# Optimization experiments

Hardware: AMD Instinct MI355X
Metric: run time of the kernel (lower is better)

The kernel has to match this reference:

```python
import jax, jax.numpy as jnp
import numpy as np

N = 100000
E = 1600000
IN_DIM, HID_DIM, OUT_DIM = 128, 64, 128


def glorot(key, shape):
    lim = float(np.sqrt(6.0 / (shape[0] + shape[1])))
    return jax.random.uniform(key, shape, jnp.float32, -lim, lim)


def setup_inputs() -> dict:
    key = jax.random.key(0)
    k1, k2, k3, k4, k5 = jax.random.split(key, 5)
    x = jax.random.normal(k1, (N, IN_DIM), jnp.float32)
    edge_index = jax.random.randint(k2, (2, E), 0, N, jnp.int64)
    edge_weight = jax.random.uniform(k3, (E,), jnp.float32)
    W1 = glorot(k4, (IN_DIM, HID_DIM))
    b1 = jnp.zeros((HID_DIM,), jnp.float32)
    W2 = glorot(k5, (HID_DIM, OUT_DIM))
    b2 = jnp.zeros((OUT_DIM,), jnp.float32)
    return {"x": x, "edge_index": edge_index, "edge_weight": edge_weight,
            "W1": W1, "b1": b1, "W2": W2, "b2": b2}


def gcn_norm(edge_index, edge_weight, num_nodes):
    # add self-loops with weight 1 (PyG GCNConv default)
    loops = jnp.arange(num_nodes, dtype=edge_index.dtype)
    row = jnp.concatenate([edge_index[0], loops])
    col = jnp.concatenate([edge_index[1], loops])
    w = jnp.concatenate([edge_weight, jnp.ones((num_nodes,), edge_weight.dtype)])
    deg = jax.ops.segment_sum(w, col, num_segments=num_nodes)  # in-degree of targets
    dinv = jnp.where(deg > 0, jax.lax.rsqrt(deg), 0.0)
    norm = dinv[row] * w * dinv[col]  # [E+N]
    return row, col, norm


def gcn_conv(x, row, col, norm, W, b, num_nodes):
    h = x @ W                                   # [N, D_out]
    msg = h[row] * norm[:, None]                # [E+N, D_out] gather + scale
    out = jax.ops.segment_sum(msg, col, num_segments=num_nodes)  # scatter-add
    return out + b


def reference(x, edge_index, edge_weight, W1, b1, W2, b2):
    row, col, norm = gcn_norm(edge_index, edge_weight, N)
    h = jax.nn.relu(gcn_conv(x, row, col, norm, W1, b1, N))
    out = gcn_conv(h, row, col, norm, W2, b2, N)
    return out
```

## Files before the change

### kernel.cpp

```cpp
#include <hip/hip_runtime.h>
#include <hip/hip_bf16.h>

typedef __hip_bfloat16 bf16;
typedef __attribute__((ext_vector_type(8))) short short8;
typedef __attribute__((ext_vector_type(4))) float f32x4;
typedef __attribute__((ext_vector_type(2))) unsigned uv2;
typedef __attribute__((ext_vector_type(4))) unsigned uv4;
union V8 { uint4 u; short8 v; };

__device__ __forceinline__ float bf2f(bf16 v) { return __bfloat162float(v); }
__device__ __forceinline__ float lo16(unsigned u) { return __uint_as_float((u & 0xffffu) << 16); }
__device__ __forceinline__ float hi16(unsigned u) { return __uint_as_float(u & 0xffff0000u); }
__device__ __forceinline__ unsigned short f2bfbits(float f) {
    return (unsigned short)(__hip_bfloat16_raw(__float2bfloat16(f)).x);
}
__device__ __forceinline__ unsigned pack2(float a, float b) {
    return (unsigned)f2bfbits(a) | ((unsigned)f2bfbits(b) << 16);
}

__device__ __forceinline__ float ldf(const void* p, size_t i, bool isbf) {
    return isbf ? bf2f(((const bf16*)p)[i]) : ((const float*)p)[i];
}
__device__ __forceinline__ int ldi(const void* p, size_t i, bool is64) {
    return is64 ? (int)((const long long*)p)[i] : ((const int*)p)[i];
}
__device__ __forceinline__ float sane(float v) {
    return (v == v && fabsf(v) < 1e30f) ? v : 0.f;
}

__device__ __forceinline__ uint2 nt_ld2(const uint2* p) {
    uv2 v = __builtin_nontemporal_load((const uv2*)p);
    return make_uint2(v.x, v.y);
}
__device__ __forceinline__ void nt_st4(uint4* p, uint4 v) {
    uv4 t; t.x = v.x; t.y = v.y; t.z = v.z; t.w = v.w;
    __builtin_nontemporal_store(t, (uv4*)p);
}

#define DC_CNT_SHIFT 44
#define DC_FIX_MASK  0xFFFFFFFFFFFULL
#define DC_FIX_SCALE 4194304.0f

__global__ void initk(unsigned long long* __restrict__ dc, int* __restrict__ hist,
                      int* __restrict__ bcnt, int n, int initdc,
                      const unsigned* __restrict__ w1w, const unsigned* __restrict__ eiw,
                      int* __restrict__ flags) {
    int i = blockIdx.x * blockDim.x + threadIdx.x;
    if (initdc && i < n) dc[i] = (unsigned long long)(1u << 22);
    if (i < 256) { hist[i] = 0; bcnt[i] = 0; }
    if (blockIdx.x == 0) {
        __shared__ int cnt[2];
        if (threadIdx.x < 2) cnt[threadIdx.x] = 0;
        __syncthreads();
        int c0 = 0;
        for (int j = threadIdx.x; j < 4096; j += 256) {
            unsigned u = w1w[j];
            unsigned e0 = (u >> 7) & 0xFFu, e1 = (u >> 23) & 0xFFu;
            if (e0 <= 125u && e1 <= 125u) c0++;
        }
        int c1 = 0;
        for (int j = threadIdx.x; j < 2048; j += 256)
            if (eiw[2 * j + 1] == 0u) c1++;
        atomicAdd(&cnt[0], c0);
        atomicAdd(&cnt[1], c1);
        __syncthreads();
        if (threadIdx.x == 0) {
            flags[0] = (cnt[0] >= 3072) ? 1 : 0;
            flags[1] = (cnt[1] >= 1024) ? 1 : 0;
        }
    }
}

__global__ void degcnt(const void* __restrict__ ei, const void* __restrict__ w,
                       unsigned long long* __restrict__ dc,
                       const int* __restrict__ flags, int e, int n) {
    const bool isbf = flags[0] != 0;
    const bool is64 = flags[1] != 0;
    int i = blockIdx.x * blockDim.x + threadIdx.x;
    if (i < e) {
        int c = ldi(ei, (size_t)e + i, is64);
        if ((unsigned)c < (unsigned)n) {
            float wv = sane(ldf(w, i, isbf));
            wv = fminf(fmaxf(wv, 0.f), 1024.f);
            unsigned long long pk = (1ULL << DC_CNT_SHIFT)
                                  + (unsigned long long)llrintf(wv * DC_FIX_SCALE);
            atomicAdd(&dc[c], pk);
        }
    }
}

__global__ __launch_bounds__(1024) void binA(const void* __restrict__ ei,
                                             const void* __restrict__ w,
                                             int* __restrict__ bcnt,
                                             uint2* __restrict__ stage,
                                             const int* __restrict__ flags,
                                             int e, int n, int k, int cap) {
    __shared__ uint2 recs[4096];
    __shared__ unsigned tgt[4096];
    __shared__ int lh[256], loff[256], lbase[256];
    const bool isbf = flags[0] != 0;
    const bool is64 = flags[1] != 0;
    const int t = threadIdx.x;
    if (t < 256) lh[t] = 0;
    __syncthreads();

    int b_[4], lr_[4], valid_[4];
    uint2 rec_[4];
    const int base = blockIdx.x * 4096;
#pragma unroll
    for (int u = 0; u < 4; ++u) {
        int i = base + u * 1024 + t;
        valid_[u] = 0;
        if (i < e) {
            int r = ldi(ei, (size_t)i, is64);
            int c = ldi(ei, (size_t)e + i, is64);
            if ((unsigned)c < (unsigned)n) {
                bool rv = (unsigned)r < (unsigned)n;
                float wv = rv ? sane(ldf(w, i, isbf)) : 0.f;
                int b = c >> k;
                unsigned cloc = (unsigned)(c - (b << k));
                rec_[u] = make_uint2((cloc << 20) | (rv ? (unsigned)r : 0u),
                                     __float_as_uint(wv));
                b_[u] = b;
                lr_[u] = atomicAdd(&lh[b], 1);
                valid_[u] = 1;
            }
        }
    }
    __syncthreads();

    if (t < 256) loff[t] = lh[t];
    __syncthreads();
    for (int off = 1; off < 256; off <<= 1) {
        int v = 0;
        if (t < 256 && t >= off) v = loff[t - off];
        __syncthreads();
        if (t < 256 && t >= off) loff[t] += v;
        __syncthreads();
    }
    if (t < 256) {
        int c = lh[t];
        loff[t] -= c;
        lbase[t] = (c > 0) ? atomicAdd(&bcnt[t], c) : 0;
    }
    __syncthreads();

#pragma unroll
    for (int u = 0; u < 4; ++u)
        if (valid_[u]) {
            int slot = loff[b_[u]] + lr_[u];
            recs[slot] = rec_[u];
            unsigned gi = (unsigned)(lbase[b_[u]] + lr_[u]);
            tgt[slot] = (gi < (unsigned)cap)
                          ? (unsigned)b_[u] * (unsigned)cap + gi
                          : 0xFFFFFFFFu;
        }
    __syncthreads();

    const int total = loff[255] + lh[255];
    for (int s = t; s < total; s += 1024) {
        unsigned g = tgt[s];
        if (g != 0xFFFFFFFFu) stage[g] = recs[s];
    }
}

__global__ __launch_bounds__(1024) void degcntB(const uint2* __restrict__ stage,
                                                const int* __restrict__ bcnt,
                                                unsigned long long* __restrict__ dc,
                                                int n, int k, int cap) {
    __shared__ unsigned long long dcl[4096];
    const int b  = blockIdx.x;
    const int lo = b << k;
    const int hi = min(n, lo + (1 << k));
    const int bs = hi - lo;
    const int t  = threadIdx.x;
    for (int j = t; j < bs; j += 1024)
        dcl[j] = (unsigned long long)(1u << 22);
    __syncthreads();
    const uint2* sb = stage + (size_t)b * cap;
    const int cnt_b = min(bcnt[b], cap);
    for (int s = t; s < cnt_b; s += 1024) {
        uint2 rec = sb[s];
        int cloc  = (int)(rec.x >> 20);
        float wv  = __uint_as_float(rec.y);
        wv = fminf(fmaxf(wv, 0.f), 1024.f);
        unsigned long long pk = (1ULL << DC_CNT_SHIFT)
                              + (unsigned long long)llrintf(wv * DC_FIX_SCALE);
        atomicAdd(&dcl[cloc], pk);
    }
    __syncthreads();
    for (int j = t; j < bs; j += 1024) dc[lo + j] = dcl[j];
}

__global__ __launch_bounds__(1024) void scan1(const unsigned long long* __restrict__ dc,
                                              int* __restrict__ rp,
                                              int* __restrict__ bsum, int n) {
    __shared__ int s[1024];
    int gid = blockIdx.x * 1024 + threadIdx.x;
    int v = (gid < n) ? (int)(dc[gid] >> DC_CNT_SHIFT) : 0;
    s[threadIdx.x] = v;
    __syncthreads();
    for (int off = 1; off < 1024; off <<= 1) {
        int t = 0;
        if (threadIdx.x >= off) t = s[threadIdx.x - off];
        __syncthreads();
        if (threadIdx.x >= off) s[threadIdx.x] += t;
        __syncthreads();
    }
    if (gid < n) rp[gid] = s[threadIdx.x] - v;
    if (threadIdx.x == 1023) bsum[blockIdx.x] = s[1023];
}

__global__ __launch_bounds__(1024) void scan2(const int* __restrict__ bsum,
                                              int* __restrict__ bsx, int nb) {
    __shared__ int s[1024];
    int v = (threadIdx.x < nb) ? bsum[threadIdx.x] : 0;
    s[threadIdx.x] = v;
    __syncthreads();
    for (int off = 1; off < 1024; off <<= 1) {
        int t = 0;
        if (threadIdx.x >= off) t = s[threadIdx.x - off];
        __syncthreads();
        if (threadIdx.x >= off) s[threadIdx.x] += t;
        __syncthreads();
    }
    if (threadIdx.x < nb) bsx[threadIdx.x] = s[threadIdx.x] - v;
}

__global__ __launch_bounds__(1024) void scan3(int* __restrict__ rp, int* __restrict__ cursor,
                                              const int* __restrict__ bsx,
                                              unsigned long long* __restrict__ dc,
                                              int* __restrict__ hist,
                                              int n, int e) {
    __shared__ int lh[256];
    const int t = threadIdx.x;
    if (t < 256) lh[t] = 0;
    __syncthreads();
    int i = blockIdx.x * 1024 + t;
    if (i < n) {
        int v = rp[i] + bsx[i >> 10];
        rp[i] = v;
        cursor[i] = v;
        unsigned long long dv = dc[i];
        int c = (int)(dv >> DC_CNT_SHIFT);
        float d = (float)(dv & DC_FIX_MASK) * (1.0f / DC_FIX_SCALE);
        float di = d > 0.f ? rsqrtf(d) : 0.f;
        dc[i] = (dv & ~DC_FIX_MASK) | (unsigned long long)__float_as_uint(di);
        atomicAdd(&lh[min(c, 255)], 1);
    }
    __syncthreads();
    if (t < 256) {
        int c = lh[t];
        if (c > 0) atomicAdd(&hist[t], c);
    }
    if (i == 0) rp[n] = e;
}

__global__ void fill(const void* __restrict__ ei, const void* __restrict__ w,
                     int* __restrict__ cursor, uint2* __restrict__ epack,
                     const int* __restrict__ flags, int e, int n) {
    const bool isbf = flags[0] != 0;
    const bool is64 = flags[1] != 0;
    int i = blockIdx.x * blockDim.x + threadIdx.x;
    if (i < e) {
        int r = ldi(ei, (size_t)i, is64);
        int c = ldi(ei, (size_t)e + i, is64);
        if ((unsigned)c < (unsigned)n) {
            bool rv = (unsigned)r < (unsigned)n;
            float wv = rv ? sane(ldf(w, i, isbf)) : 0.f;
            int pos = atomicAdd(&cursor[c], 1);
            epack[pos] = make_uint2(rv ? (unsigned)r : 0u, __float_as_uint(wv));
        }
    }
}

__global__ __launch_bounds__(1024) void fillB(const int* __restrict__ rp,
                                              const uint2* __restrict__ stage,
                                              const int* __restrict__ bcnt,
                                              uint2* __restrict__ epack,
                                              int n, int k, int cap) {
    __shared__ int ncur[4096];
    const int b  = blockIdx.x;
    const int lo = b << k;
    const int hi = min(n, lo + (1 << k));
    const int t  = threadIdx.x;
    for (int j = t; j < hi - lo; j += 1024) ncur[j] = rp[lo + j];
    __syncthreads();
    const uint2* sb = stage + (size_t)b * cap;
    const int cnt_b = min(bcnt[b], cap);
    for (int s = t; s < cnt_b; s += 1024) {
        uint2 rec = sb[s];
        int cloc  = (int)(rec.x >> 20);
        unsigned r = rec.x & 0xFFFFFu;
        int pos = atomicAdd(&ncur[cloc], 1);
        epack[pos] = make_uint2(r, rec.y);
    }
}

__global__ void hscan(const int* __restrict__ hist, int* __restrict__ hcur) {
    __shared__ int s[256];
    int v = hist[threadIdx.x];
    s[threadIdx.x] = v;
    __syncthreads();
    for (int off = 1; off < 256; off <<= 1) {
        int t = 0;
        if (threadIdx.x >= off) t = s[threadIdx.x - off];
        __syncthreads();
        if (threadIdx.x >= off) s[threadIdx.x] += t;
        __syncthreads();
    }
    hcur[threadIdx.x] = s[threadIdx.x] - v;
}

__global__ __launch_bounds__(1024) void sortk(const unsigned long long* __restrict__ dc,
                                              int* __restrict__ hcur,
                                              int* __restrict__ order, int n) {
    __shared__ int lh[256];
    __shared__ int lbase[256];
    const int t = threadIdx.x;
    for (int b = t; b < 256; b += 1024) lh[b] = 0;
    __syncthreads();
    const int i = blockIdx.x * 1024 + t;
    int b = 0, lrank = 0;
    if (i < n) {
        b = min((int)(dc[i] >> DC_CNT_SHIFT), 255);
        lrank = atomicAdd(&lh[b], 1);
    }
    __syncthreads();
    for (int bb = t; bb < 256; bb += 1024) {
        int c = lh[bb];
        lbase[bb] = (c > 0) ? atomicAdd(&hcur[bb], c) : 0;
    }
    __syncthreads();
    if (i < n) order[lbase[b] + lrank] = i;
}

__global__ __launch_bounds__(256) void gemm1_mfma(const void* __restrict__ x,
                                                  const void* __restrict__ W1,
                                                  const float* __restrict__ dinvp,
                                                  const int* __restrict__ flags,
                                                  unsigned short* __restrict__ G1,
                                                  int n) {
    const bool isbf = flags[0] != 0;
    __shared__ uint4 bfr[16 * 64];
    for (int idx = threadIdx.x; idx < 16 * 64; idx += 256) {
        int lane = idx & 63, fr = idx >> 6;
        int ct = fr >> 2, ks = fr & 3;
        int k0 = ks * 32 + (lane >> 4) * 8;
        int col = ct * 16 + (lane & 15);
        unsigned short h[8];
#pragma unroll
        for (int j = 0; j < 8; ++j)
            h[j] = f2bfbits(ldf(W1, (size_t)(k0 + j) * 64 + col, isbf));
        bfr[idx] = make_uint4((unsigned)h[0] | ((unsigned)h[1] << 16),
                              (unsigned)h[2] | ((unsigned)h[3] << 16),
                              (unsigned)h[4] | ((unsigned)h[5] << 16),
                              (unsigned)h[6] | ((unsigned)h[7] << 16));
    }
    __syncthreads();

    const int lane = threadIdx.x & 63;
    const int m = lane & 15, q = lane >> 4;
    const int wid = (blockIdx.x * 256 + threadIdx.x) >> 6;
    const int nw  = (gridDim.x * 256) >> 6;
    const int nchunk = (n + 15) >> 4;

    for (int ch = wid; ch < nchunk; ch += nw) {
        const int row0 = ch * 16;
        const int rA = min(row0 + m, n - 1);
        V8 a[4];
        if (isbf) {
            const uint4* xr = (const uint4*)((const bf16*)x + (size_t)rA * 128);
#pragma unroll
            for (int ks = 0; ks < 4; ++ks) a[ks].u = xr[ks * 4 + q];
        } else {
            const float4* xr4 = (const float4*)((const float*)x + (size_t)rA * 128);
#pragma unroll
            for (int ks = 0; ks < 4; ++ks) {
                float4 v0 = xr4[ks * 8 + q * 2];
                float4 v1 = xr4[ks * 8 + q * 2 + 1];
                a[ks].u = make_uint4(pack2(v0.x, v0.y), pack2(v0.z, v0.w),
                                     pack2(v1.x, v1.y), pack2(v1.z, v1.w));
            }
        }
#pragma unroll
        for (int ct = 0; ct < 4; ++ct) {
            f32x4 acc = {0.f, 0.f, 0.f, 0.f};
#pragma unroll
            for (int ks = 0; ks < 4; ++ks) {
                V8 b; b.u = bfr[(ct * 4 + ks) * 64 + lane];
                acc = __builtin_amdgcn_mfma_f32_16x16x32_bf16(a[ks].v, b.v, acc, 0, 0, 0);
            }
#pragma unroll
            for (int r = 0; r < 4; ++r) {
                int row = row0 + q * 4 + r;
                if (row < n)
                    G1[(size_t)row * 64 + ct * 16 + m] = f2bfbits(dinvp[2 * (size_t)row] * acc[r]);
            }
        }
    }
}

__device__ __forceinline__ void gacc8(const int* __restrict__ rp,
                                      const uint2* __restrict__ epack,
                                      const uint4* __restrict__ Gv,
                                      int node, int sub, float acc[8]) {
    uint4 self = Gv[(size_t)node * 8 + sub];
    acc[0] = lo16(self.x); acc[1] = hi16(self.x);
    acc[2] = lo16(self.y); acc[3] = hi16(self.y);
    acc[4] = lo16(self.z); acc[5] = hi16(self.z);
    acc[6] = lo16(self.w); acc[7] = hi16(self.w);

    const int s0 = rp[node], s1 = rp[node + 1];
    const uint2 fb = make_uint2((unsigned)node, 0u);
    int idx = s0 + sub;
    uint2 ld = (idx < s1) ? nt_ld2(&epack[idx]) : fb;
    for (int base = s0; base < s1; base += 8) {
        int nidx = base + 8 + sub;
        uint2 nld = (nidx < s1) ? nt_ld2(&epack[nidx]) : fb;
        int rr[8]; float wv[8];
#pragma unroll
        for (int u = 0; u < 8; ++u) {
            rr[u] = __shfl((int)ld.x, u, 8);
            wv[u] = __uint_as_float((unsigned)__shfl((int)ld.y, u, 8));
        }
        uint4 gp[8];
#pragma unroll
        for (int u = 0; u < 8; ++u) gp[u] = Gv[(size_t)rr[u] * 8 + sub];
#pragma unroll
        for (int u = 0; u < 8; ++u) {
            acc[0] = fmaf(wv[u], lo16(gp[u].x), acc[0]);
            acc[1] = fmaf(wv[u], hi16(gp[u].x), acc[1]);
            acc[2] = fmaf(wv[u], lo16(gp[u].y), acc[2]);
            acc[3] = fmaf(wv[u], hi16(gp[u].y), acc[3]);
            acc[4] = fmaf(wv[u], lo16(gp[u].z), acc[4]);
            acc[5] = fmaf(wv[u], hi16(gp[u].z), acc[5]);
            acc[6] = fmaf(wv[u], lo16(gp[u].w), acc[6]);
            acc[7] = fmaf(wv[u], hi16(gp[u].w), acc[7]);
        }
        ld = nld;
    }
}

__global__ __launch_bounds__(256, 4) void agg1(const int* __restrict__ rp,
                                               const uint2* __restrict__ epack,
                                               const int* __restrict__ order,
                                               const uint4* __restrict__ G1v,
                                               const float* __restrict__ dinvp,
                                               const void* __restrict__ b1,
                                               const int* __restrict__ flags,
                                               uint4* __restrict__ G2v, int n) {
    const bool isbf = flags[0] != 0;
    const int sub = threadIdx.x & 7;
    const int g   = (blockIdx.x * 256 + threadIdx.x) >> 3;
    if (g >= n) return;
    const int node = order[g];

    float acc[8];
    gacc8(rp, epack, G1v, node, sub, acc);

    const float dv = dinvp[2 * (size_t)node];
    unsigned o[4];
#pragma unroll
    for (int t = 0; t < 4; ++t) {
        float h0 = dv * acc[2 * t]     + ldf(b1, 8 * sub + 2 * t, isbf);
        float h1 = dv * acc[2 * t + 1] + ldf(b1, 8 * sub + 2 * t + 1, isbf);
        h0 = h0 > 0.f ? h0 : 0.f;
        h1 = h1 > 0.f ? h1 : 0.f;
        o[t] = pack2(dv * h0, dv * h1);
    }
    nt_st4(&G2v[(size_t)node * 8 + sub], make_uint4(o[0], o[1], o[2], o[3]));
}

__global__ __launch_bounds__(256, 4) void agg2(const int* __restrict__ rp,
                                               const uint2* __restrict__ epack,
                                               const int* __restrict__ order,
                                               const uint4* __restrict__ G2v,
                                               const float* __restrict__ dinvp,
                                               uint4* __restrict__ Tv, int n) {
    const int sub = threadIdx.x & 7;
    const int g   = (blockIdx.x * 256 + threadIdx.x) >> 3;
    if (g >= n) return;
    const int node = order[g];

    float acc[8];
    gacc8(rp, epack, G2v, node, sub, acc);

    const float dv = dinvp[2 * (size_t)node];
    uint4 o;
    o.x = pack2(dv * acc[0], dv * acc[1]);
    o.y = pack2(dv * acc[2], dv * acc[3]);
    o.z = pack2(dv * acc[4], dv * acc[5]);
    o.w = pack2(dv * acc[6], dv * acc[7]);
    nt_st4(&Tv[(size_t)node * 8 + sub], o);
}

__global__ __launch_bounds__(256) void outgemm_mfma(const bf16* __restrict__ T,
                                                    const void* __restrict__ W2,
                                                    const void* __restrict__ b2,
                                                    const int* __restrict__ flags,
                                                    void* __restrict__ outp, int n) {
    const bool isbf = flags[0] != 0;
    __shared__ uint4 bfr[16 * 64];
    __shared__ float b2s[128];
    for (int idx = threadIdx.x; idx < 16 * 64; idx += 256) {
        int lane = idx & 63, fr = idx >> 6;
        int ct = fr >> 1, ks = fr & 1;
        int k0 = ks * 32 + (lane >> 4) * 8;
        int col = ct * 16 + (lane & 15);
        unsigned short h[8];
#pragma unroll
        for (int j = 0; j < 8; ++j)
            h[j] = f2bfbits(ldf(W2, (size_t)(k0 + j) * 128 + col, isbf));
        bfr[idx] = make_uint4((unsigned)h[0] | ((unsigned)h[1] << 16),
                              (unsigned)h[2] | ((unsigned)h[3] << 16),
                              (unsigned)h[4] | ((unsigned)h[5] << 16),
                              (unsigned)h[6] | ((unsigned)h[7] << 16));
    }
    for (int i = threadIdx.x; i < 128; i += 256) b2s[i] = ldf(b2, i, isbf);
    __syncthreads();

    const int lane = threadIdx.x & 63;
    const int m = lane & 15, q = lane >> 4;
    const int wid = (blockIdx.x * 256 + threadIdx.x) >> 6;
    const int nw  = (gridDim.x * 256) >> 6;
    const int nchunk = (n + 15) >> 4;

    for (int ch = wid; ch < nchunk; ch += nw) {
        const int row0 = ch * 16;
        const int rA = min(row0 + m, n - 1);
        const uint4* tr = (const uint4*)(T + (size_t)rA * 64);
        V8 a[2];
        a[0].u = tr[q];
        a[1].u = tr[4 + q];
#pragma unroll
        for (int ct = 0; ct < 8; ++ct) {
            f32x4 acc = {0.f, 0.f, 0.f, 0.f};
#pragma unroll
            for (int ks = 0; ks < 2; ++ks) {
                V8 b; b.u = bfr[(ct * 2 + ks) * 64 + lane];
                acc = __builtin_amdgcn_mfma_f32_16x16x32_bf16(a[ks].v, b.v, acc, 0, 0, 0);
            }
            const int col = ct * 16 + m;
            const float bb = b2s[col];
#pragma unroll
            for (int r = 0; r < 4; ++r) {
                int row = row0 + q * 4 + r;
                if (row < n) {
                    float o = acc[r] + bb;
                    if (isbf) ((bf16*)outp)[(size_t)row * 128 + col] = __float2bfloat16(o);
                    else      ((float*)outp)[(size_t)row * 128 + col] = o;
                }
            }
        }
    }
}

extern "C" void kernel_launch(void* const* d_in, const int* in_sizes, int n_in,
                              void* d_out, int out_size, void* d_ws, size_t ws_size,
                              hipStream_t stream) {
    const void* x  = d_in[0];
    const void* ei = d_in[1];
    const void* ew = d_in[2];
    const void* W1 = d_in[3];
    const void* b1 = d_in[4];
    const void* W2 = d_in[5];
    const void* b2 = d_in[6];

    const int n = in_sizes[0] / 128;
    const int e = in_sizes[2];
    const int nb = (n + 1023) / 1024;

    int*   flags  = (int*)d_ws;
    unsigned long long* dc = (unsigned long long*)((int*)d_ws + 8);
    int*   rp     = (int*)d_ws + 8 + 2 * (size_t)n;
    int*   cursor = rp + n + 1;
    int*   bsum   = cursor + n;
    int*   bsx    = bsum + 1024;
    int*   hist   = bsum + 512;
    int*   hcur   = bsx + 512;
    int*   bcnt   = bsx + 256;
    int*   order  = cursor;
    size_t w_off  = (size_t)(8 + 4 * (size_t)n + 1 + 2048);
    w_off = (w_off + 3) & ~(size_t)3;
    uint2*    epack = (uint2*)((int*)d_ws + w_off);
    size_t g_off = w_off + 2 * (size_t)e;
    g_off = (g_off + 3) & ~(size_t)3;
    unsigned* G1 = (unsigned*)d_ws + g_off;
    unsigned* G2 = G1 + (size_t)n * 32;

    const float* dinvp = (const float*)dc;
    uint2* stage = (uint2*)G1;

    int bs0 = (n + 255) / 256;
    int k = 0;
    while ((1 << k) < bs0) ++k;
    int beff = (n + (1 << k) - 1) >> k;
    int cap  = (int)((32 * (size_t)n) / (size_t)beff);
    size_t mean = ((size_t)e + beff - 1) / beff;
    bool fastfill = (n <= (1 << 18)) && (k <= 12) &&
                    ((size_t)cap >= mean + mean / 2 + 1024);

    const int nchunk = (n + 15) >> 4;
    int ggrid = (nchunk + 3) / 4;
    if (ggrid > 2048) ggrid = 2048;
    if (ggrid < 192)  ggrid = 192;

    initk<<<(n + 255) / 256, 256, 0, stream>>>(dc, hist, bcnt, n, fastfill ? 0 : 1,
                                               (const unsigned*)W1, (const unsigned*)ei, flags);
    if (fastfill) {
        binA<<<(e + 4095) / 4096, 1024, 0, stream>>>(ei, ew, bcnt, stage, flags, e, n, k, cap);
        degcntB<<<beff, 1024, 0, stream>>>(stage, bcnt, dc, n, k, cap);
    } else {
        degcnt<<<(e + 255) / 256, 256, 0, stream>>>(ei, ew, dc, flags, e, n);
    }
    scan1<<<nb, 1024, 0, stream>>>(dc, rp, bsum, n);
    scan2<<<1, 1024, 0, stream>>>(bsum, bsx, nb);
    scan3<<<nb, 1024, 0, stream>>>(rp, cursor, bsx, dc, hist, n, e);
    if (fastfill) {
        fillB<<<beff, 1024, 0, stream>>>(rp, stage, bcnt, epack, n, k, cap);
    } else {
        fill<<<(e + 255) / 256, 256, 0, stream>>>(ei, ew, cursor, epack, flags, e, n);
    }
    hscan<<<1, 256, 0, stream>>>(hist, hcur);
    sortk<<<nb, 1024, 0, stream>>>(dc, hcur, order, n);

    gemm1_mfma<<<ggrid, 256, 0, stream>>>(x, W1, dinvp, flags, (unsigned short*)G1, n);
    agg1<<<(n * 8 + 255) / 256, 256, 0, stream>>>(rp, epack, order, (const uint4*)G1,
                                                  dinvp, b1, flags, (uint4*)G2, n);
    agg2<<<(n * 8 + 255) / 256, 256, 0, stream>>>(rp, epack, order, (const uint4*)G2,
                                                  dinvp, (uint4*)G1, n);
    outgemm_mfma<<<ggrid, 256, 0, stream>>>((const bf16*)G1, W2, b2, flags, d_out, n);
}
```

Measured before the change: 350.6 us.

## Fuse second aggregation with output GEMM through shared-memory tiles

Merges the agg2 gather-aggregation and the output MFMA GEMM into one persistent kernel. Each block aggregates 32 nodes into LDS, then runs the 16x16x32 bf16 MFMA on them and scatters the output rows by node id. This removes the round trip of the intermediate T array through global memory and one launch. In exchange each tile needs block-wide barriers, the grid is capped at 1024 blocks, and output writes are no longer row-contiguous. Two smaller changes ride along: scan1 reads only the high 32-bit word of each degree counter, and initk launches a single block when the fast-fill path is used.

```diff
diff --git a/kernel.cpp b/kernel.cpp
--- a/kernel.cpp
+++ b/kernel.cpp
@@ -197,7 +197,7 @@
                                               int* __restrict__ bsum, int n) {
     __shared__ int s[1024];
     int gid = blockIdx.x * 1024 + threadIdx.x;
-    int v = (gid < n) ? (int)(dc[gid] >> DC_CNT_SHIFT) : 0;
+    int v = (gid < n) ? (int)(((const unsigned*)dc)[2 * (size_t)gid + 1] >> (DC_CNT_SHIFT - 32)) : 0;
     s[threadIdx.x] = v;
     __syncthreads();
     for (int off = 1; off < 1024; off <<= 1) {
@@ -472,37 +472,20 @@
     nt_st4(&G2v[(size_t)node * 8 + sub], make_uint4(o[0], o[1], o[2], o[3]));
 }
 
-__global__ __launch_bounds__(256, 4) void agg2(const int* __restrict__ rp,
-                                               const uint2* __restrict__ epack,
-                                               const int* __restrict__ order,
-                                               const uint4* __restrict__ G2v,
-                                               const float* __restrict__ dinvp,
-                                               uint4* __restrict__ Tv, int n) {
-    const int sub = threadIdx.x & 7;
-    const int g   = (blockIdx.x * 256 + threadIdx.x) >> 3;
-    if (g >= n) return;
-    const int node = order[g];
-
-    float acc[8];
-    gacc8(rp, epack, G2v, node, sub, acc);
-
-    const float dv = dinvp[2 * (size_t)node];
-    uint4 o;
-    o.x = pack2(dv * acc[0], dv * acc[1]);
-    o.y = pack2(dv * acc[2], dv * acc[3]);
-    o.z = pack2(dv * acc[4], dv * acc[5]);
-    o.w = pack2(dv * acc[6], dv * acc[7]);
-    nt_st4(&Tv[(size_t)node * 8 + sub], o);
-}
-
-__global__ __launch_bounds__(256) void outgemm_mfma(const bf16* __restrict__ T,
-                                                    const void* __restrict__ W2,
-                                                    const void* __restrict__ b2,
-                                                    const int* __restrict__ flags,
-                                                    void* __restrict__ outp, int n) {
+__global__ __launch_bounds__(256, 4) void agg2out(const int* __restrict__ rp,
+                                                  const uint2* __restrict__ epack,
+                                                  const int* __restrict__ order,
+                                                  const uint4* __restrict__ G2v,
+                                                  const float* __restrict__ dinvp,
+                                                  const void* __restrict__ W2,
+                                                  const void* __restrict__ b2,
+                                                  const int* __restrict__ flags,
+                                                  void* __restrict__ outp, int n) {
     const bool isbf = flags[0] != 0;
     __shared__ uint4 bfr[16 * 64];
     __shared__ float b2s[128];
+    __shared__ uint4 tls[32 * 8];
+    __shared__ int   nds[32];
     for (int idx = threadIdx.x; idx < 16 * 64; idx += 256) {
         int lane = idx & 63, fr = idx >> 6;
         int ct = fr >> 1, ks = fr & 1;
@@ -520,39 +503,59 @@
     for (int i = threadIdx.x; i < 128; i += 256) b2s[i] = ldf(b2, i, isbf);
     __syncthreads();
 
+    const int sub  = threadIdx.x & 7;
+    const int lg   = threadIdx.x >> 3;
     const int lane = threadIdx.x & 63;
     const int m = lane & 15, q = lane >> 4;
-    const int wid = (blockIdx.x * 256 + threadIdx.x) >> 6;
-    const int nw  = (gridDim.x * 256) >> 6;
-    const int nchunk = (n + 15) >> 4;
-
-    for (int ch = wid; ch < nchunk; ch += nw) {
-        const int row0 = ch * 16;
-        const int rA = min(row0 + m, n - 1);
-        const uint4* tr = (const uint4*)(T + (size_t)rA * 64);
-        V8 a[2];
-        a[0].u = tr[q];
-        a[1].u = tr[4 + q];
-#pragma unroll
-        for (int ct = 0; ct < 8; ++ct) {
-            f32x4 acc = {0.f, 0.f, 0.f, 0.f};
-#pragma unroll
-            for (int ks = 0; ks < 2; ++ks) {
-                V8 b; b.u = bfr[(ct * 2 + ks) * 64 + lane];
-                acc = __builtin_amdgcn_mfma_f32_16x16x32_bf16(a[ks].v, b.v, acc, 0, 0, 0);
-            }
+    const int wid = threadIdx.x >> 6;
+    const int ntile = (n + 31) >> 5;
+
+    for (int tile = blockIdx.x; tile < ntile; tile += gridDim.x) {
+        const int g = tile * 32 + lg;
+        uint4 o = make_uint4(0u, 0u, 0u, 0u);
+        int node = 0;
+        if (g < n) {
+            node = order[g];
+            float acc[8];
+            gacc8(rp, epack, G2v, node, sub, acc);
+            const float dv = dinvp[2 * (size_t)node];
+            o.x = pack2(dv * acc[0], dv * acc[1]);
+            o.y = pack2(dv * acc[2], dv * acc[3]);
+            o.z = pack2(dv * acc[4], dv * acc[5]);
+            o.w = pack2(dv * acc[6], dv * acc[7]);
+        }
+        tls[lg * 8 + sub] = o;
+        if (sub == 0) nds[lg] = node;
+        __syncthreads();
+
+        const int chunk = wid >> 1;
+        const int lrow  = chunk * 16 + m;
+        V8 a0, a1;
+        a0.u = tls[lrow * 8 + q];
+        a1.u = tls[lrow * 8 + 4 + q];
+#pragma unroll
+        for (int c8 = 0; c8 < 4; ++c8) {
+            const int ct = (wid & 1) * 4 + c8;
+            f32x4 acc4 = {0.f, 0.f, 0.f, 0.f};
+            V8 b0; b0.u = bfr[(ct * 2 + 0) * 64 + lane];
+            acc4 = __builtin_amdgcn_mfma_f32_16x16x32_bf16(a0.v, b0.v, acc4, 0, 0, 0);
+            V8 b1; b1.u = bfr[(ct * 2 + 1) * 64 + lane];
+            acc4 = __builtin_amdgcn_mfma_f32_16x16x32_bf16(a1.v, b1.v, acc4, 0, 0, 0);
             const int col = ct * 16 + m;
             const float bb = b2s[col];
 #pragma unroll
             for (int r = 0; r < 4; ++r) {
-                int row = row0 + q * 4 + r;
-                if (row < n) {
-                    float o = acc[r] + bb;
-                    if (isbf) ((bf16*)outp)[(size_t)row * 128 + col] = __float2bfloat16(o);
-                    else      ((float*)outp)[(size_t)row * 128 + col] = o;
+                int lr = chunk * 16 + q * 4 + r;
+                int gg = tile * 32 + lr;
+                if (gg < n) {
+                    float ov = acc4[r] + bb;
+                    int nd = nds[lr];
+                    if (isbf) ((bf16*)outp)[(size_t)nd * 128 + col] = __float2bfloat16(ov);
+                    else      ((float*)outp)[(size_t)nd * 128 + col] = ov;
                 }
             }
         }
+        __syncthreads();
     }
 }
 
@@ -606,8 +609,9 @@
     if (ggrid > 2048) ggrid = 2048;
     if (ggrid < 192)  ggrid = 192;
 
-    initk<<<(n + 255) / 256, 256, 0, stream>>>(dc, hist, bcnt, n, fastfill ? 0 : 1,
-                                               (const unsigned*)W1, (const unsigned*)ei, flags);
+    initk<<<fastfill ? 1 : (n + 255) / 256, 256, 0, stream>>>(
+        dc, hist, bcnt, n, fastfill ? 0 : 1,
+        (const unsigned*)W1, (const unsigned*)ei, flags);
     if (fastfill) {
         binA<<<(e + 4095) / 4096, 1024, 0, stream>>>(ei, ew, bcnt, stage, flags, e, n, k, cap);
         degcntB<<<beff, 1024, 0, stream>>>(stage, bcnt, dc, n, k, cap);
@@ -628,7 +632,8 @@
     gemm1_mfma<<<ggrid, 256, 0, stream>>>(x, W1, dinvp, flags, (unsigned short*)G1, n);
     agg1<<<(n * 8 + 255) / 256, 256, 0, stream>>>(rp, epack, order, (const uint4*)G1,
                                                   dinvp, b1, flags, (uint4*)G2, n);
-    agg2<<<(n * 8 + 255) / 256, 256, 0, stream>>>(rp, epack, order, (const uint4*)G2,
-                                                  dinvp, (uint4*)G1, n);
-    outgemm_mfma<<<ggrid, 256, 0, stream>>>((const bf16*)G1, W2, b2, flags, d_out, n);
-}
+    int a2grid = (n + 31) / 32;
+    if (a2grid > 1024) a2grid = 1024;
+    agg2out<<<a2grid, 256, 0, stream>>>(rp, epack, order, (const uint4*)G2,
+                                        dinvp, W2, b2, flags, d_out, n);
+}
```

Result: faster. 337.7 us (-3.7%).
